# Optimization experiments

Measured on AMD Instinct MI355X. Metric: run time of the kernel, lower is better.

Reference implementation:

```python
import jax, jax.numpy as jnp
import numpy as np

VOCAB = 50000
EMB = 128
HID = 256
OUT = 1


def setup_inputs() -> dict:
    key = jax.random.key(0)
    ks = jax.random.split(key, 8)
    B, T = 256, 512
    s_emb = 1.0 / np.sqrt(EMB)
    s_hid = 1.0 / np.sqrt(HID)
    return {
        "x": jax.random.randint(ks[0], (B, T), 0, VOCAB, dtype=jnp.int32),
        "emb_table": jax.random.normal(ks[1], (VOCAB, EMB), dtype=jnp.float32),
        "W_ih": jax.random.uniform(ks[2], (4 * HID, EMB), jnp.float32, -s_hid, s_hid),
        "W_hh": jax.random.uniform(ks[3], (4 * HID, HID), jnp.float32, -s_hid, s_hid),
        "b_ih": jax.random.uniform(ks[4], (4 * HID,), jnp.float32, -s_hid, s_hid),
        "b_hh": jax.random.uniform(ks[5], (4 * HID,), jnp.float32, -s_hid, s_hid),
        "W_fc": jax.random.uniform(ks[6], (OUT, HID), jnp.float32, -s_hid, s_hid),
        "b_fc": jax.random.uniform(ks[7], (OUT,), jnp.float32, -s_hid, s_hid),
    }


def _lstm_last_hidden(embedded, W_ih, W_hh, b_ih, b_hh):
    # embedded: [B, T, E]; PyTorch gate order: i, f, g, o
    B = embedded.shape[0]
    H = W_hh.shape[1]
    # precompute input projections for all timesteps: [T, B, 4H]
    x_proj = jnp.einsum('bte,ge->tbg', embedded, W_ih) + b_ih + b_hh

    def step(carry, xp):
        h, c = carry
        gates = xp + h @ W_hh.T  # [B, 4H]
        i, f, g, o = jnp.split(gates, 4, axis=-1)
        i = jax.nn.sigmoid(i)
        f = jax.nn.sigmoid(f)
        g = jnp.tanh(g)
        o = jax.nn.sigmoid(o)
        c = f * c + i * g
        h = o * jnp.tanh(c)
        return (h, c), None

    h0 = jnp.zeros((B, H), embedded.dtype)
    c0 = jnp.zeros((B, H), embedded.dtype)
    (h_last, _), _ = jax.lax.scan(step, (h0, c0), x_proj)
    return h_last  # [B, H] == lstm_out[:, -1, :]


def reference(x, emb_table, W_ih, W_hh, b_ih, b_hh, W_fc, b_fc):
    embedded = emb_table[x]  # [B, T, E]
    h_last = _lstm_last_hidden(embedded, W_ih, W_hh, b_ih, b_hh)
    logits = h_last @ W_fc.T + b_fc  # [B, OUT]
    return jax.nn.sigmoid(logits)
```

## Files before the change

kernel.cpp:

```cpp
#include <hip/hip_runtime.h>
#include <hip/hip_bf16.h>
#include <stdint.h>

#define VOCAB 50000
#define EMB   128
#define HID   256
#define G4    1024
#define BATCH 256
#define SEQ   512
#define LOG2E 1.4426950408889634f

typedef __attribute__((ext_vector_type(8))) short bf16x8;
typedef __attribute__((ext_vector_type(4))) float f32x4;
typedef __attribute__((ext_vector_type(4))) int   i32x4;
typedef __attribute__((ext_vector_type(2))) unsigned u32x2;

__device__ __forceinline__ ushort f2bf(float f) {
  uint32_t u; __builtin_memcpy(&u, &f, 4);
  uint32_t r = (u + 0x7fffu + ((u >> 16) & 1u)) >> 16;
  return (ushort)r;
}
__device__ __forceinline__ float asf(uint32_t x) {
  float f; __builtin_memcpy(&f, &x, 4);
  return f;
}
__device__ __forceinline__ float rcp(float x) { return __builtin_amdgcn_rcpf(x); }
__device__ __forceinline__ float ex2(float x) { return __builtin_amdgcn_exp2f(x); }

#define WAIT_LGKM() asm volatile("s_waitcnt lgkmcnt(0)" ::: "memory")
#define RAW_BAR()  do { __builtin_amdgcn_sched_barrier(0); \
                        __builtin_amdgcn_s_barrier(); \
                        __builtin_amdgcn_sched_barrier(0); } while (0)

__global__ __launch_bounds__(256) void k_proj(
    const float* __restrict__ emb, const float* __restrict__ W_ih,
    const float* __restrict__ b_ih, const float* __restrict__ b_hh,
    ushort* __restrict__ proj) {
  const int lane = threadIdx.x & 63;
  const int wv = threadIdx.x >> 6;
  const int vbase = (blockIdx.x * 4 + wv) * 64;
  const int lm = lane & 15, lq = lane >> 4;

  bf16x8 A[4][4];
  #pragma unroll
  for (int mt = 0; mt < 4; ++mt) {
    int v = vbase + mt * 16 + lm;
    int vc = v < VOCAB ? v : 0;
    const float* rp = emb + (size_t)vc * EMB;
    #pragma unroll
    for (int kt = 0; kt < 4; ++kt) {
      const float* p = rp + kt * 32 + lq * 8;
      #pragma unroll
      for (int i = 0; i < 8; ++i) A[mt][kt][i] = (short)f2bf(p[i]);
    }
  }
  for (int nt = 0; nt < 64; ++nt) {
    const int g = nt * 16 + lm;
    const int newcol = (g & 255) * 4 + (g >> 8);
    bf16x8 B[4];
    #pragma unroll
    for (int kt = 0; kt < 4; ++kt) {
      const float* p = W_ih + (size_t)g * EMB + kt * 32 + lq * 8;
      #pragma unroll
      for (int i = 0; i < 8; ++i) B[kt][i] = (short)f2bf(p[i]);
    }
    const float bias = b_ih[g] + b_hh[g];
    #pragma unroll
    for (int mt = 0; mt < 4; ++mt) {
      f32x4 acc = {0.f, 0.f, 0.f, 0.f};
      #pragma unroll
      for (int kt = 0; kt < 4; ++kt)
        acc = __builtin_amdgcn_mfma_f32_16x16x32_bf16(A[mt][kt], B[kt], acc, 0, 0, 0);
      #pragma unroll
      for (int r = 0; r < 4; ++r) {
        int row = vbase + mt * 16 + lq * 4 + r;
        if (row < VOCAB) proj[(size_t)row * G4 + newcol] = f2bf((acc[r] + bias) * LOG2E);
      }
    }
  }
}

__global__ __launch_bounds__(256) void k_w2(const float* __restrict__ Whh,
                                            int* __restrict__ W2) {
  const int f = blockIdx.x * 256 + threadIdx.x;
  const int lane = f & 63, kc = (f >> 6) & 3, nt = (f >> 8) & 7, wv = (f >> 11) & 7;
  const int grow = (nt >> 1) * 256 + wv * 32 + (nt & 1) * 16 + (lane & 15);
  const int k0 = kc * 64 + (lane >> 4) * 16;
  const float* src = Whh + (size_t)grow * HID + k0;
  unsigned d[4];
  #pragma unroll
  for (int dw = 0; dw < 4; ++dw) {
    unsigned acc = 0;
    #pragma unroll
    for (int b = 0; b < 4; ++b) {
      int q = (int)rintf(src[dw * 4 + b] * 2032.f);
      q = q > 127 ? 127 : (q < -127 ? -127 : q);
      acc |= ((unsigned)q & 0xffu) << (8 * b);
    }
    d[dw] = acc;
  }
  i32x4 o = {(int)d[0], (int)d[1], (int)d[2], (int)d[3]};
  *(i32x4*)(W2 + (size_t)f * 4) = o;
}

__global__ __launch_bounds__(512, 2) void k_lstm(
    const int* __restrict__ x, const ushort* __restrict__ proj,
    const int* __restrict__ W2, const float* __restrict__ W_fc,
    const float* __restrict__ b_fc, float* __restrict__ out) {
  __shared__ __align__(16) char hbuf[2][16 * 256];
  __shared__ __align__(16) int xlds[SEQ * 2];
  __shared__ float red[8][2];

  const int tid = threadIdx.x;
  const int lane = tid & 63, wv = tid >> 6;
  const int lm = lane & 15, lq = lane >> 4;
  const int b0 = blockIdx.x * 2;
  const int js = (lane >> 4) & 1;
  const int b = lane >> 5;
  const int jme = wv * 32 + js * 16 + lm;
  const int bpaddr = (((lane >> 5) << 4) | lm) * 4;

  i32x4 Wf[8][4];
  {
    const i32x4* wb = (const i32x4*)W2;
    #pragma unroll
    for (int nt = 0; nt < 8; ++nt)
      #pragma unroll
      for (int kc = 0; kc < 4; ++kc)
        Wf[nt][kc] = wb[wv * 2048 + nt * 256 + kc * 64 + lane];
    #pragma unroll
    for (int nt = 0; nt < 8; ++nt)
      #pragma unroll
      for (int kc = 0; kc < 4; ++kc)
        asm volatile("" : "+a"(Wf[nt][kc]));
  }

  for (int i = tid; i < SEQ * 2; i += 512) {
    int bl = i >> 9, t = i & 511;
    xlds[t * 2 + bl] = x[(b0 + bl) * SEQ + t];
  }
  for (int i = tid; i < 2048; i += 512) ((int*)hbuf)[i] = 0;

  float c = 0.f, hl = 0.f;

  __syncthreads();

  u32x2 xp;
  {
    int i0 = xlds[b];
    xp = *(const u32x2*)(proj + (size_t)i0 * G4 + jme * 4);
  }

  const float S2 = LOG2E / 258064.f;

  int cur = 0;
  #pragma clang loop unroll(disable)
  for (int t = 0; t < SEQ; ++t) {
    const int nxt = cur ^ 1;

    i32x4 acc[8];
    #pragma unroll
    for (int nt = 0; nt < 8; ++nt) acc[nt] = (i32x4){0, 0, 0, 0};

    if (t > 0) {
      i32x4 A[4];
      #pragma unroll
      for (int kc = 0; kc < 4; ++kc) {
        int byte = (lm * 256 + kc * 64 + lq * 16) ^ ((lm & 7) << 4);
        A[kc] = *(const i32x4*)(hbuf[cur] + byte);
      }
      #pragma unroll
      for (int kc = 0; kc < 4; ++kc)
        #pragma unroll
        for (int nt = 0; nt < 8; ++nt)
          acc[nt] = __builtin_amdgcn_mfma_i32_16x16x64_i8(A[kc], Wf[nt][kc], acc[nt], 0, 0, 0);
    }

    float gv[4];
    #pragma unroll
    for (int g = 0; g < 4; ++g) {
      int v0 = __builtin_amdgcn_ds_bpermute(bpaddr, acc[g * 2 + 0][0]);
      int v1 = __builtin_amdgcn_ds_bpermute(bpaddr, acc[g * 2 + 1][0]);
      int av = js ? v1 : v0;
      unsigned w = (g < 2) ? xp[0] : xp[1];
      unsigned bits = (g & 1) ? (w & 0xffff0000u) : (w << 16);
      gv[g] = (float)av * S2 + asf(bits);
    }

    if (t + 1 < SEQ) {
      int idx = xlds[(t + 1) * 2 + b];
      xp = *(const u32x2*)(proj + (size_t)idx * G4 + jme * 4);
    }

    {
      float si = rcp(1.f + ex2(-gv[0]));
      float sf = rcp(1.f + ex2(-gv[1]));
      float eg = ex2(gv[2] + gv[2]);
      float tg = (eg - 1.f) * rcp(eg + 1.f);
      float so = rcp(1.f + ex2(-gv[3]));
      float cn = sf * c + si * tg;
      c = cn;
      float e2 = ex2(cn * (2.f * LOG2E));
      float h = so - (so + so) * rcp(e2 + 1.f);
      hl = h;
      int q = (int)rintf(h * 127.f);
      int byte = (b * 1024 + jme) ^ (b * 64);
      hbuf[nxt][byte] = (char)q;
    }

    WAIT_LGKM();
    RAW_BAR();
    cur = nxt;
  }

  float p = hl * W_fc[jme];
  p += __shfl_xor(p, 1);
  p += __shfl_xor(p, 2);
  p += __shfl_xor(p, 4);
  p += __shfl_xor(p, 8);
  p += __shfl_xor(p, 16);
  if ((lane & 31) == 0) red[wv][b] = p;
  __syncthreads();
  if (tid < 2) {
    float s = 0.f;
    #pragma unroll
    for (int w = 0; w < 8; ++w) s += red[w][tid];
    s += b_fc[0];
    out[b0 + tid] = rcp(1.f + ex2(-s * LOG2E));
  }
}

extern "C" void kernel_launch(void* const* d_in, const int* in_sizes, int n_in,
                              void* d_out, int out_size, void* d_ws, size_t ws_size,
                              hipStream_t stream) {
  const int*   x    = (const int*)d_in[0];
  const float* emb  = (const float*)d_in[1];
  const float* W_ih = (const float*)d_in[2];
  const float* W_hh = (const float*)d_in[3];
  const float* b_ih = (const float*)d_in[4];
  const float* b_hh = (const float*)d_in[5];
  const float* W_fc = (const float*)d_in[6];
  const float* b_fc = (const float*)d_in[7];
  float* out = (float*)d_out;

  char* ws = (char*)d_ws;
  ushort* proj = (ushort*)ws;
  int*    W2   = (int*)(ws + 102400000);

  k_proj<<<dim3(196), dim3(256), 0, stream>>>(emb, W_ih, b_ih, b_hh, proj);
  k_w2<<<dim3(64), dim3(256), 0, stream>>>(W_hh, W2);
  k_lstm<<<dim3(128), dim3(512), 0, stream>>>(x, proj, W2, W_fc, b_fc, out);
}
```

Before: 572.9 us.

## Split recurrent MFMAs to overlap gate math, shrink h buffer, split proj grid

The LSTM step now issues the i/f gate MFMAs first, computes those sigmoids, then issues the g/o MFMAs, so transcendental work can overlap matrix-unit latency. The hidden-state LDS buffer is compacted from a 16-row swizzled layout to two padded 272-byte rows, with lanes selecting their batch row, which cuts LDS footprint and zeroing. The projection kernel grid is doubled in y so each block computes half the gate columns, for more parallelism in the precompute. Correctness relies on the MFMA A-operand rows beyond the two batch rows being ignored.

```diff
diff --git a/kernel.cpp b/kernel.cpp
--- a/kernel.cpp
+++ b/kernel.cpp
@@ -40,6 +40,7 @@
   const int wv = threadIdx.x >> 6;
   const int vbase = (blockIdx.x * 4 + wv) * 64;
   const int lm = lane & 15, lq = lane >> 4;
+  const int nt0 = blockIdx.y * 32;
 
   bf16x8 A[4][4];
   #pragma unroll
@@ -54,8 +55,8 @@
       for (int i = 0; i < 8; ++i) A[mt][kt][i] = (short)f2bf(p[i]);
     }
   }
-  for (int nt = 0; nt < 64; ++nt) {
-    const int g = nt * 16 + lm;
+  for (int ntl = 0; ntl < 32; ++ntl) {
+    const int g = (nt0 + ntl) * 16 + lm;
     const int newcol = (g & 255) * 4 + (g >> 8);
     bf16x8 B[4];
     #pragma unroll
@@ -107,7 +108,7 @@
     const int* __restrict__ x, const ushort* __restrict__ proj,
     const int* __restrict__ W2, const float* __restrict__ W_fc,
     const float* __restrict__ b_fc, float* __restrict__ out) {
-  __shared__ __align__(16) char hbuf[2][16 * 256];
+  __shared__ __align__(16) char hbuf[2][544];
   __shared__ __align__(16) int xlds[SEQ * 2];
   __shared__ float red[8][2];
 
@@ -118,6 +119,7 @@
   const int js = (lane >> 4) & 1;
   const int b = lane >> 5;
   const int jme = wv * 32 + js * 16 + lm;
+  const int bsel = (lm >> 2) & 1;
   const int bpaddr = (((lane >> 5) << 4) | lm) * 4;
 
   i32x4 Wf[8][4];
@@ -139,7 +141,7 @@
     int bl = i >> 9, t = i & 511;
     xlds[t * 2 + bl] = x[(b0 + bl) * SEQ + t];
   }
-  for (int i = tid; i < 2048; i += 512) ((int*)hbuf)[i] = 0;
+  for (int i = tid; i < 272; i += 512) ((int*)hbuf)[i] = 0;
 
   float c = 0.f, hl = 0.f;
 
@@ -162,29 +164,51 @@
     #pragma unroll
     for (int nt = 0; nt < 8; ++nt) acc[nt] = (i32x4){0, 0, 0, 0};
 
+    i32x4 A[4];
     if (t > 0) {
-      i32x4 A[4];
-      #pragma unroll
-      for (int kc = 0; kc < 4; ++kc) {
-        int byte = (lm * 256 + kc * 64 + lq * 16) ^ ((lm & 7) << 4);
-        A[kc] = *(const i32x4*)(hbuf[cur] + byte);
-      }
+      const char* hb = hbuf[cur];
+      #pragma unroll
+      for (int kc = 0; kc < 4; ++kc)
+        A[kc] = *(const i32x4*)(hb + bsel * 272 + kc * 64 + lq * 16);
       #pragma unroll
       for (int kc = 0; kc < 4; ++kc)
         #pragma unroll
-        for (int nt = 0; nt < 8; ++nt)
+        for (int nt = 0; nt < 4; ++nt)
           acc[nt] = __builtin_amdgcn_mfma_i32_16x16x64_i8(A[kc], Wf[nt][kc], acc[nt], 0, 0, 0);
     }
 
-    float gv[4];
-    #pragma unroll
-    for (int g = 0; g < 4; ++g) {
-      int v0 = __builtin_amdgcn_ds_bpermute(bpaddr, acc[g * 2 + 0][0]);
-      int v1 = __builtin_amdgcn_ds_bpermute(bpaddr, acc[g * 2 + 1][0]);
-      int av = js ? v1 : v0;
-      unsigned w = (g < 2) ? xp[0] : xp[1];
-      unsigned bits = (g & 1) ? (w & 0xffff0000u) : (w << 16);
-      gv[g] = (float)av * S2 + asf(bits);
+    float gv0, gv1;
+    {
+      int v0 = __builtin_amdgcn_ds_bpermute(bpaddr, acc[0][0]);
+      int v1 = __builtin_amdgcn_ds_bpermute(bpaddr, acc[1][0]);
+      int v2 = __builtin_amdgcn_ds_bpermute(bpaddr, acc[2][0]);
+      int v3 = __builtin_amdgcn_ds_bpermute(bpaddr, acc[3][0]);
+      int ai = js ? v1 : v0;
+      int af = js ? v3 : v2;
+      gv0 = (float)ai * S2 + asf(xp[0] << 16);
+      gv1 = (float)af * S2 + asf(xp[0] & 0xffff0000u);
+    }
+    float si = rcp(1.f + ex2(-gv0));
+    float sf = rcp(1.f + ex2(-gv1));
+
+    if (t > 0) {
+      #pragma unroll
+      for (int kc = 0; kc < 4; ++kc)
+        #pragma unroll
+        for (int nt = 4; nt < 8; ++nt)
+          acc[nt] = __builtin_amdgcn_mfma_i32_16x16x64_i8(A[kc], Wf[nt][kc], acc[nt], 0, 0, 0);
+    }
+
+    float gv2, gv3;
+    {
+      int v4 = __builtin_amdgcn_ds_bpermute(bpaddr, acc[4][0]);
+      int v5 = __builtin_amdgcn_ds_bpermute(bpaddr, acc[5][0]);
+      int v6 = __builtin_amdgcn_ds_bpermute(bpaddr, acc[6][0]);
+      int v7 = __builtin_amdgcn_ds_bpermute(bpaddr, acc[7][0]);
+      int ag = js ? v5 : v4;
+      int ao = js ? v7 : v6;
+      gv2 = (float)ag * S2 + asf(xp[1] << 16);
+      gv3 = (float)ao * S2 + asf(xp[1] & 0xffff0000u);
     }
 
     if (t + 1 < SEQ) {
@@ -193,19 +217,16 @@
     }
 
     {
-      float si = rcp(1.f + ex2(-gv[0]));
-      float sf = rcp(1.f + ex2(-gv[1]));
-      float eg = ex2(gv[2] + gv[2]);
+      float eg = ex2(gv2 + gv2);
       float tg = (eg - 1.f) * rcp(eg + 1.f);
-      float so = rcp(1.f + ex2(-gv[3]));
+      float so = rcp(1.f + ex2(-gv3));
       float cn = sf * c + si * tg;
       c = cn;
       float e2 = ex2(cn * (2.f * LOG2E));
       float h = so - (so + so) * rcp(e2 + 1.f);
       hl = h;
       int q = (int)rintf(h * 127.f);
-      int byte = (b * 1024 + jme) ^ (b * 64);
-      hbuf[nxt][byte] = (char)q;
+      hbuf[nxt][b * 272 + jme] = (char)q;
     }
 
     WAIT_LGKM();
@@ -247,7 +268,7 @@
   ushort* proj = (ushort*)ws;
   int*    W2   = (int*)(ws + 102400000);
 
-  k_proj<<<dim3(196), dim3(256), 0, stream>>>(emb, W_ih, b_ih, b_hh, proj);
+  k_proj<<<dim3(196, 2), dim3(256), 0, stream>>>(emb, W_ih, b_ih, b_hh, proj);
   k_w2<<<dim3(64), dim3(256), 0, stream>>>(W_hh, W2);
   k_lstm<<<dim3(128), dim3(512), 0, stream>>>(x, proj, W2, W_fc, b_fc, out);
 }
```

After: 551.1 us. 3.8% less time.

## Interleave per-gate MFMA with activations, shrink h buffer, prefetch two steps ahead

Applied to the files above, without the earlier changes.

The LSTM recurrence now computes each gate pair's MFMAs separately and starts its activation before the next gate's MFMAs, so transcendental math can overlap matrix work. The h buffer is shrunk to two padded rows per batch (only 2 batch rows are real), and the projection gather is prefetched two timesteps ahead using two alternating registers with a manually unrolled loop. The projection kernel's grid is split over gate columns in a second dimension to double parallelism. Risks include higher register pressure from the unroll and a changed LDS layout for A-fragment loads.

```diff
diff --git a/kernel.cpp b/kernel.cpp
--- a/kernel.cpp
+++ b/kernel.cpp
@@ -40,6 +40,7 @@
   const int wv = threadIdx.x >> 6;
   const int vbase = (blockIdx.x * 4 + wv) * 64;
   const int lm = lane & 15, lq = lane >> 4;
+  const int nt0 = blockIdx.y * 32;
 
   bf16x8 A[4][4];
   #pragma unroll
@@ -54,8 +55,8 @@
       for (int i = 0; i < 8; ++i) A[mt][kt][i] = (short)f2bf(p[i]);
     }
   }
-  for (int nt = 0; nt < 64; ++nt) {
-    const int g = nt * 16 + lm;
+  for (int ntl = 0; ntl < 32; ++ntl) {
+    const int g = (nt0 + ntl) * 16 + lm;
     const int newcol = (g & 255) * 4 + (g >> 8);
     bf16x8 B[4];
     #pragma unroll
@@ -107,7 +108,7 @@
     const int* __restrict__ x, const ushort* __restrict__ proj,
     const int* __restrict__ W2, const float* __restrict__ W_fc,
     const float* __restrict__ b_fc, float* __restrict__ out) {
-  __shared__ __align__(16) char hbuf[2][16 * 256];
+  __shared__ __align__(16) char hbuf[2][544];
   __shared__ __align__(16) int xlds[SEQ * 2];
   __shared__ float red[8][2];
 
@@ -118,6 +119,7 @@
   const int js = (lane >> 4) & 1;
   const int b = lane >> 5;
   const int jme = wv * 32 + js * 16 + lm;
+  const int bsel = (lm >> 2) & 1;
   const int bpaddr = (((lane >> 5) << 4) | lm) * 4;
 
   i32x4 Wf[8][4];
@@ -139,79 +141,84 @@
     int bl = i >> 9, t = i & 511;
     xlds[t * 2 + bl] = x[(b0 + bl) * SEQ + t];
   }
-  for (int i = tid; i < 2048; i += 512) ((int*)hbuf)[i] = 0;
+  for (int i = tid; i < 272; i += 512) ((int*)hbuf)[i] = 0;
 
   float c = 0.f, hl = 0.f;
 
   __syncthreads();
 
-  u32x2 xp;
+  u32x2 xp0, xp1;
   {
     int i0 = xlds[b];
-    xp = *(const u32x2*)(proj + (size_t)i0 * G4 + jme * 4);
+    xp0 = *(const u32x2*)(proj + (size_t)i0 * G4 + jme * 4);
+    int i1 = xlds[2 + b];
+    xp1 = *(const u32x2*)(proj + (size_t)i1 * G4 + jme * 4);
   }
 
   const float S2 = LOG2E / 258064.f;
 
-  int cur = 0;
+#define GATE_PHASE(G, DOMFMA, XP, GV)                                         \
+  {                                                                           \
+    i32x4 a0 = {0, 0, 0, 0}, a1 = {0, 0, 0, 0};                               \
+    if (DOMFMA) {                                                             \
+      _Pragma("unroll")                                                       \
+      for (int kc = 0; kc < 4; ++kc) {                                        \
+        a0 = __builtin_amdgcn_mfma_i32_16x16x64_i8(A[kc], Wf[2*(G)][kc], a0, 0, 0, 0);   \
+        a1 = __builtin_amdgcn_mfma_i32_16x16x64_i8(A[kc], Wf[2*(G)+1][kc], a1, 0, 0, 0); \
+      }                                                                       \
+    }                                                                         \
+    int v0 = __builtin_amdgcn_ds_bpermute(bpaddr, a0[0]);                     \
+    int v1 = __builtin_amdgcn_ds_bpermute(bpaddr, a1[0]);                     \
+    int av = js ? v1 : v0;                                                    \
+    unsigned w_ = ((G) < 2) ? XP[0] : XP[1];                                  \
+    unsigned bits_ = ((G) & 1) ? (w_ & 0xffff0000u) : (w_ << 16);             \
+    GV = (float)av * S2 + asf(bits_);                                         \
+  }
+
+#define STEP(T, RB, WB, DOMFMA, XP)                                           \
+  {                                                                           \
+    i32x4 A[4];                                                               \
+    if (DOMFMA) {                                                             \
+      const char* hb_ = hbuf[RB];                                             \
+      _Pragma("unroll")                                                       \
+      for (int kc = 0; kc < 4; ++kc)                                          \
+        A[kc] = *(const i32x4*)(hb_ + bsel * 272 + kc * 64 + lq * 16);        \
+    }                                                                         \
+    float gv_;                                                                \
+    GATE_PHASE(2, DOMFMA, XP, gv_);                               \
+    float eg_ = ex2(gv_ + gv_);                                               \
+    float tg_ = (eg_ - 1.f) * rcp(eg_ + 1.f);                                 \
+    GATE_PHASE(0, DOMFMA, XP, gv_);                               \
+    float si_ = rcp(1.f + ex2(-gv_));                                         \
+    float sitg_ = si_ * tg_;                                                  \
+    GATE_PHASE(1, DOMFMA, XP, gv_);                               \
+    float sf_ = rcp(1.f + ex2(-gv_));                                         \
+    float cn_ = sf_ * c + sitg_;                                              \
+    c = cn_;                                                                  \
+    float e2_ = ex2(cn_ * (2.f * LOG2E));                                     \
+    float tc_ = 1.f - 2.f * rcp(e2_ + 1.f);                      \
+    GATE_PHASE(3, DOMFMA, XP, gv_);                               \
+    float so_ = rcp(1.f + ex2(-gv_));                                         \
+    float h_ = so_ * tc_;                                                     \
+    hl = h_;                                                                  \
+    int q_ = (int)rintf(h_ * 127.f);                                          \
+    hbuf[WB][b * 272 + jme] = (char)q_;                                       \
+    {                                                     \
+      int t2_ = ((T) + 2 < SEQ) ? (T) + 2 : SEQ - 1;                          \
+      int idx_ = xlds[t2_ * 2 + b];                                           \
+      XP = *(const u32x2*)(proj + (size_t)idx_ * G4 + jme * 4);               \
+    }                                                                         \
+    WAIT_LGKM();                                                              \
+    RAW_BAR();                                                                \
+  }
+
+  STEP(0, 0, 1, false, xp0);
   #pragma clang loop unroll(disable)
-  for (int t = 0; t < SEQ; ++t) {
-    const int nxt = cur ^ 1;
-
-    i32x4 acc[8];
-    #pragma unroll
-    for (int nt = 0; nt < 8; ++nt) acc[nt] = (i32x4){0, 0, 0, 0};
-
-    if (t > 0) {
-      i32x4 A[4];
-      #pragma unroll
-      for (int kc = 0; kc < 4; ++kc) {
-        int byte = (lm * 256 + kc * 64 + lq * 16) ^ ((lm & 7) << 4);
-        A[kc] = *(const i32x4*)(hbuf[cur] + byte);
-      }
-      #pragma unroll
-      for (int kc = 0; kc < 4; ++kc)
-        #pragma unroll
-        for (int nt = 0; nt < 8; ++nt)
-          acc[nt] = __builtin_amdgcn_mfma_i32_16x16x64_i8(A[kc], Wf[nt][kc], acc[nt], 0, 0, 0);
-    }
-
-    float gv[4];
-    #pragma unroll
-    for (int g = 0; g < 4; ++g) {
-      int v0 = __builtin_amdgcn_ds_bpermute(bpaddr, acc[g * 2 + 0][0]);
-      int v1 = __builtin_amdgcn_ds_bpermute(bpaddr, acc[g * 2 + 1][0]);
-      int av = js ? v1 : v0;
-      unsigned w = (g < 2) ? xp[0] : xp[1];
-      unsigned bits = (g & 1) ? (w & 0xffff0000u) : (w << 16);
-      gv[g] = (float)av * S2 + asf(bits);
-    }
-
-    if (t + 1 < SEQ) {
-      int idx = xlds[(t + 1) * 2 + b];
-      xp = *(const u32x2*)(proj + (size_t)idx * G4 + jme * 4);
-    }
-
-    {
-      float si = rcp(1.f + ex2(-gv[0]));
-      float sf = rcp(1.f + ex2(-gv[1]));
-      float eg = ex2(gv[2] + gv[2]);
-      float tg = (eg - 1.f) * rcp(eg + 1.f);
-      float so = rcp(1.f + ex2(-gv[3]));
-      float cn = sf * c + si * tg;
-      c = cn;
-      float e2 = ex2(cn * (2.f * LOG2E));
-      float h = so - (so + so) * rcp(e2 + 1.f);
-      hl = h;
-      int q = (int)rintf(h * 127.f);
-      int byte = (b * 1024 + jme) ^ (b * 64);
-      hbuf[nxt][byte] = (char)q;
-    }
-
-    WAIT_LGKM();
-    RAW_BAR();
-    cur = nxt;
-  }
+  for (int tt = 0; tt < 255; ++tt) {
+    STEP(2 * tt + 1, 1, 0, true, xp1);
+    STEP(2 * tt + 2, 0, 1, true, xp0);
+  }
+  STEP(511, 1, 0, true, xp1);
 
   float p = hl * W_fc[jme];
   p += __shfl_xor(p, 1);
@@ -247,7 +254,7 @@
   ushort* proj = (ushort*)ws;
   int*    W2   = (int*)(ws + 102400000);
 
-  k_proj<<<dim3(196), dim3(256), 0, stream>>>(emb, W_ih, b_ih, b_hh, proj);
+  k_proj<<<dim3(196, 2), dim3(256), 0, stream>>>(emb, W_ih, b_ih, b_hh, proj);
   k_w2<<<dim3(64), dim3(256), 0, stream>>>(W_hh, W2);
   k_lstm<<<dim3(128), dim3(512), 0, stream>>>(x, proj, W2, W_fc, b_fc, out);
 }
```

Result: faster. 522.6 us (-8.8%).
